# Performance work log

Measured on AMD Instinct MI355X. Metric: run time of the kernel, lower is better.

## Reference

```python
import jax, jax.numpy as jnp
import numpy as np

N_FFT = 4096
N_STAGES = 3
N_CHUNKS = 2 ** N_STAGES


def _mod_seq(order):
    mset = [0]
    for o in range(order):
        step = 2 ** o
        mset = [x + d for x in mset for d in (0, step)]
    return mset


def _perm_matrix(N, order):
    m = np.zeros((N, N), dtype=np.float32)
    base = 2 ** order
    k = 0
    for p in _mod_seq(order):
        for j in range(N // base):
            m[j * base + p, k] = 1.0
            k += 1
    return m


def setup_inputs() -> dict:
    key = jax.random.key(0)
    x = jax.random.normal(key, (8, 512, N_FFT), dtype=jnp.float32)
    perm = jnp.asarray(_perm_matrix(N_FFT, N_STAGES))
    return {"x": x, "perm": perm}


def reference(x, perm):
    # y[..., k] = sum_i x[..., i] * perm[i, k]  (dense matmul by one-hot permutation)
    y = jnp.matmul(x, perm)  # [B, T, N_FFT]
    return tuple(jnp.split(y, N_CHUNKS, axis=-1))  # N_CHUNKS arrays of [B, T, N_FFT // N_CHUNKS]
```

## Files before the change

### kernel.cpp

```cpp
#include <hip/hip_runtime.h>


#define NFFT        4096
#define BT          (8 * 512)
#define CHUNK_ELEMS (BT * 512)
#define TOTAL_COLS  (BT * 512)
#define THREADS     (TOTAL_COLS / 4)

__global__ __launch_bounds__(256) void
FFTPermuter_2748779070248_kernel(const float4* __restrict__ x4,
                                 float4* __restrict__ out4) {
    const int g = blockIdx.x * blockDim.x + threadIdx.x;

    float f[32];
#pragma unroll
    for (int m = 0; m < 8; ++m) {
        float4 t = x4[(size_t)g * 8 + m];
        f[4 * m + 0] = t.x;
        f[4 * m + 1] = t.y;
        f[4 * m + 2] = t.z;
        f[4 * m + 3] = t.w;
    }

    const int ms[8] = {0, 4, 2, 6, 1, 5, 3, 7};
#pragma unroll
    for (int c = 0; c < 8; ++c) {
        const int p = ms[c];
        float4 o;
        o.x = f[0 * 8 + p];
        o.y = f[1 * 8 + p];
        o.z = f[2 * 8 + p];
        o.w = f[3 * 8 + p];
        out4[(size_t)c * (CHUNK_ELEMS / 4) + g] = o;
    }
}

extern "C" void kernel_launch(void* const* d_in, const int* in_sizes, int n_in,
                              void* d_out, int out_size, void* d_ws, size_t ws_size,
                              hipStream_t stream) {
    const float4* x4   = (const float4*)d_in[0];
    float4*       out4 = (float4*)d_out;

    const int threads = THREADS;
    const int block   = 256;
    const int grid    = threads / block;
    FFTPermuter_2748779070248_kernel<<<grid, block, 0, stream>>>(x4, out4);
}
```

Before: 157.8 us.

## Stage input tile through LDS for fully coalesced loads and stores

Each block now loads a contiguous 8192-float tile with fully coalesced float4 reads, scatters the values into a phase-major shared-memory layout, then reads contiguous float4s per chunk to write coalesced outputs. The old version had each thread read 128 contiguous bytes, which gave strided per-instruction access across the wavefront. The cost is 32KB of LDS per block, a barrier, possible bank conflicts on the scalar LDS writes, and lower occupancy.

```diff
diff --git a/kernel.cpp b/kernel.cpp
--- a/kernel.cpp
+++ b/kernel.cpp
@@ -1,37 +1,39 @@
 #include <hip/hip_runtime.h>
 
 
-#define NFFT        4096
-#define BT          (8 * 512)
-#define CHUNK_ELEMS (BT * 512)
-#define TOTAL_COLS  (BT * 512)
-#define THREADS     (TOTAL_COLS / 4)
+#define COLS_TOTAL  (8u * 512u * 512u)
+#define TILE_COLS   1024
+#define BLOCK       256
 
-__global__ __launch_bounds__(256) void
+__global__ __launch_bounds__(BLOCK) void
 FFTPermuter_2748779070248_kernel(const float4* __restrict__ x4,
                                  float4* __restrict__ out4) {
-    const int g = blockIdx.x * blockDim.x + threadIdx.x;
+    __shared__ __align__(16) float lds[8 * TILE_COLS];
 
-    float f[32];
+    const int    tid   = threadIdx.x;
+    const size_t tile  = blockIdx.x;
+    const size_t base4 = tile * 2048;
+
 #pragma unroll
-    for (int m = 0; m < 8; ++m) {
-        float4 t = x4[(size_t)g * 8 + m];
-        f[4 * m + 0] = t.x;
-        f[4 * m + 1] = t.y;
-        f[4 * m + 2] = t.z;
-        f[4 * m + 3] = t.w;
+    for (int k = 0; k < 8; ++k) {
+        const int e4 = k * BLOCK + tid;
+        float4 v = x4[base4 + e4];
+        const int col = e4 >> 1;
+        const int ph0 = (e4 & 1) * 4;
+        lds[(ph0 + 0) * TILE_COLS + col] = v.x;
+        lds[(ph0 + 1) * TILE_COLS + col] = v.y;
+        lds[(ph0 + 2) * TILE_COLS + col] = v.z;
+        lds[(ph0 + 3) * TILE_COLS + col] = v.w;
     }
+    __syncthreads();
 
     const int ms[8] = {0, 4, 2, 6, 1, 5, 3, 7};
+    const size_t colbase4 = tile * (TILE_COLS / 4);
 #pragma unroll
     for (int c = 0; c < 8; ++c) {
         const int p = ms[c];
-        float4 o;
-        o.x = f[0 * 8 + p];
-        o.y = f[1 * 8 + p];
-        o.z = f[2 * 8 + p];
-        o.w = f[3 * 8 + p];
-        out4[(size_t)c * (CHUNK_ELEMS / 4) + g] = o;
+        const float4 o = *(const float4*)&lds[p * TILE_COLS + 4 * tid];
+        out4[(size_t)c * (COLS_TOTAL / 4) + colbase4 + tid] = o;
     }
 }
 
@@ -41,8 +43,6 @@
     const float4* x4   = (const float4*)d_in[0];
     float4*       out4 = (float4*)d_out;
 
-    const int threads = THREADS;
-    const int block   = 256;
-    const int grid    = threads / block;
-    FFTPermuter_2748779070248_kernel<<<grid, block, 0, stream>>>(x4, out4);
+    const int grid = COLS_TOTAL / TILE_COLS;
+    FFTPermuter_2748779070248_kernel<<<grid, BLOCK, 0, stream>>>(x4, out4);
 }
```

Result: no change. 155.1 us (-1.7%).
